# Kernel optimization log

Hardware: AMD Instinct MI355X
Metric: run time of the kernel (lower is better)

## Reference

```python
import jax, jax.numpy as jnp
import numpy as np

DIM = 128
DIM_HEAD = 32
HEADS = 4
EPS = 1e-12  # F.normalize eps


def _l2_normalize(t, axis=-1):
    # matches torch F.normalize(p=2): x / max(||x||, eps)
    n = jnp.sqrt(jnp.sum(t * t, axis=axis, keepdims=True))
    return t / jnp.maximum(n, EPS)


def _dwconv3x3(x_nhwc, k_hwio, c):
    # depthwise 3x3, stride 1, SAME padding, no bias
    return jax.lax.conv_general_dilated(
        x_nhwc, k_hwio, window_strides=(1, 1), padding='SAME',
        dimension_numbers=('NHWC', 'HWIO', 'NHWC'), feature_group_count=c)


def setup_inputs() -> dict:
    key = jax.random.key(0)
    ks = jax.random.split(key, 10)
    b, h, w = 4, 256, 256
    inner = DIM_HEAD * HEADS  # == DIM
    s = 0.02
    return {
        'x': jax.random.normal(ks[0], (b, h, w, DIM), jnp.float32),
        'illumination_feature': jax.random.uniform(ks[1], (b, h, w, inner), jnp.float32),
        'Wq': jax.random.normal(ks[2], (DIM, inner), jnp.float32) * s,  # stored (in,out)
        'Wk': jax.random.normal(ks[3], (DIM, inner), jnp.float32) * s,
        'Wv': jax.random.normal(ks[4], (DIM, inner), jnp.float32) * s,
        'rescale': jnp.ones((HEADS, 1, 1), jnp.float32),
        'Wp': jax.random.normal(ks[5], (inner, DIM), jnp.float32) * s,
        'bp': jnp.zeros((DIM,), jnp.float32),
        'pe_w1': jax.random.normal(ks[6], (3, 3, 1, DIM), jnp.float32) * s,  # HWIO depthwise
        'pe_w2': jax.random.normal(ks[7], (3, 3, 1, DIM), jnp.float32) * s,
    }


def reference(x, illumination_feature, Wq, Wk, Wv, rescale, Wp, bp, pe_w1, pe_w2):
    b, h, w, c = x.shape
    n = h * w
    heads = rescale.shape[0]
    xf = x.reshape(b, n, c)
    ilf = illumination_feature.reshape(b, n, -1)

    q_inp = xf @ Wq  # [b,n,heads*d]
    k_inp = xf @ Wk
    v_inp = xf @ Wv

    def to_heads(t):  # b n (h d) -> b h n d
        return t.reshape(b, n, heads, -1).transpose(0, 2, 1, 3)

    q = to_heads(q_inp)
    k = to_heads(k_inp)
    v = to_heads(v_inp) * to_heads(ilf)  # illumination gating

    # transpose to channel attention layout: b h d n
    q = q.transpose(0, 1, 3, 2)
    k = k.transpose(0, 1, 3, 2)
    v = v.transpose(0, 1, 3, 2)

    q = _l2_normalize(q, axis=-1)
    k = _l2_normalize(k, axis=-1)

    attn = jnp.einsum('bhdn,bhen->bhde', k, q) * rescale  # [b,h,d,d]
    attn = jax.nn.softmax(attn, axis=-1)
    out = jnp.einsum('bhde,bhen->bhdn', attn, v)  # [b,h,d,n]

    # b h d n -> b n (h d)
    out = out.transpose(0, 3, 1, 2).reshape(b, n, -1)
    x1 = (out @ Wp + bp).reshape(b, h, w, c)

    # positional branch: depthwise conv -> GELU -> depthwise conv on v_inp (NHWC)
    v_img = v_inp.reshape(b, h, w, -1)
    x2 = _dwconv3x3(v_img, pe_w1, c)
    x2 = jax.nn.gelu(x2, approximate=False)
    x2 = _dwconv3x3(x2, pe_w2, c)

    return x1 + x2
```

## Files before the change

### kernel.cpp

```cpp
#include <hip/hip_runtime.h>
#include <math.h>

#define B_ 4
#define C_ 128
#define H_ 256
#define W_ 256
#define NPIX (H_*W_)
#define HEADS_ 4

typedef unsigned int uint;
typedef unsigned short ushort;
typedef __attribute__((ext_vector_type(8))) __bf16 bf16x8;
typedef __attribute__((ext_vector_type(4))) float f32x4;

__device__ __forceinline__ ushort f2bf(float f){
    uint u = __builtin_bit_cast(uint, f);
    u += 0x7FFFu + ((u>>16)&1u);
    return (ushort)(u>>16);
}
__device__ __forceinline__ float bf2f(ushort h){
    uint u = ((uint)h)<<16;
    return __builtin_bit_cast(float, u);
}
__device__ __forceinline__ int swz3(int i){ return (i ^ (i>>3)) & 7; }

__global__ __launch_bounds__(256) void k1_syrk(const float* __restrict__ x, float* __restrict__ S){
    __shared__ __align__(16) char sm[128*256];
    int blk = blockIdx.x;
    int b = blk >> 7;
    int chunk = blk & 127;
    long base = ((long)b*NPIX + (long)chunk*512) * C_;
    int t = threadIdx.x;
    int lane = t & 63;
    int w = t >> 6;
    int m0 = (w>>1)*64, n0 = (w&1)*64;

    f32x4 acc[4][4];
    #pragma unroll
    for(int i=0;i<4;i++)
        #pragma unroll
        for(int j=0;j<4;j++) acc[i][j] = {0.f,0.f,0.f,0.f};

    for(int tile=0; tile<4; ++tile){
        {
            int rp = (t>>5)*2;
            int c0 = (t&31)*4;
            const float* xp = x + base + (long)tile*128*C_;
            #pragma unroll
            for(int p=0;p<8;p++){
                int r = p*16 + rp;
                float4 a0 = *(const float4*)(xp + r*C_ + c0);
                float4 a1 = *(const float4*)(xp + (r+1)*C_ + c0);
                float v0[4] = {a0.x,a0.y,a0.z,a0.w};
                float v1[4] = {a1.x,a1.y,a1.z,a1.w};
                #pragma unroll
                for(int i=0;i<4;i++){
                    int cch = c0+i;
                    uint pk = (uint)f2bf(v0[i]) | ((uint)f2bf(v1[i])<<16);
                    *(uint*)(sm + cch*256 + ((2*r) ^ (swz3(cch)<<4))) = pk;
                }
            }
        }
        __syncthreads();
        #pragma unroll
        for(int kk=0;kk<4;kk++){
            int rb = kk*32 + (lane>>4)*8;
            bf16x8 A[4], Bf[4];
            #pragma unroll
            for(int i=0;i<4;i++){
                int cch = m0 + i*16 + (lane&15);
                A[i] = *(const bf16x8*)(sm + cch*256 + ((2*rb) ^ (swz3(cch)<<4)));
            }
            #pragma unroll
            for(int j=0;j<4;j++){
                int cch = n0 + j*16 + (lane&15);
                Bf[j] = *(const bf16x8*)(sm + cch*256 + ((2*rb) ^ (swz3(cch)<<4)));
            }
            #pragma unroll
            for(int i=0;i<4;i++)
                #pragma unroll
                for(int j=0;j<4;j++)
                    acc[i][j] = __builtin_amdgcn_mfma_f32_16x16x32_bf16(A[i], Bf[j], acc[i][j], 0,0,0);
        }
        __syncthreads();
    }
    float* Sb = S + b*C_*C_;
    int rq = (lane>>4)*4;
    int cc = lane&15;
    #pragma unroll
    for(int i=0;i<4;i++)
        #pragma unroll
        for(int j=0;j<4;j++)
            #pragma unroll
            for(int rg=0;rg<4;rg++){
                int row = m0 + i*16 + rq + rg;
                int col = n0 + j*16 + cc;
                atomicAdd(&Sb[row*C_ + col], acc[i][j][rg]);
            }
}

__global__ __launch_bounds__(256) void k2_vinp(const float* __restrict__ x, const float* __restrict__ Wv,
                                               ushort* __restrict__ vout){
    __shared__ __align__(16) char smx[128*256];
    __shared__ __align__(16) char smw[128*256];
    int blk = blockIdx.x;
    int b = blk >> 9; int tileI = blk & 511;
    long rowbase = (long)b*NPIX + (long)tileI*128;
    int t = threadIdx.x, lane = t&63, w = t>>6;
    int m0 = (w>>1)*64, n0 = (w&1)*64;

    {
        #pragma unroll
        for(int p=0;p<16;p++){
            int in = p*8 + (t>>5);
            int o0 = (t&31)*4;
            float4 wv = *(const float4*)(Wv + in*C_ + o0);
            float vv[4]={wv.x,wv.y,wv.z,wv.w};
            #pragma unroll
            for(int i=0;i<4;i++){
                int o = o0+i;
                *(ushort*)(smw + o*256 + ((2*in) ^ (swz3(o)<<4))) = f2bf(vv[i]);
            }
        }
    }
    {
        const float* xp = x + rowbase*C_;
        #pragma unroll
        for(int p=0;p<16;p++){
            int r = p*8 + (t>>5);
            int c0 = (t&31)*4;
            float4 a = *(const float4*)(xp + r*C_ + c0);
            uint2 pk;
            pk.x = (uint)f2bf(a.x) | ((uint)f2bf(a.y)<<16);
            pk.y = (uint)f2bf(a.z) | ((uint)f2bf(a.w)<<16);
            *(uint2*)(smx + r*256 + ((2*c0) ^ (swz3(r)<<4))) = pk;
        }
    }
    __syncthreads();

    f32x4 acc[4][4];
    #pragma unroll
    for(int i=0;i<4;i++)
        #pragma unroll
        for(int j=0;j<4;j++) acc[i][j] = {0.f,0.f,0.f,0.f};

    #pragma unroll
    for(int kk=0;kk<4;kk++){
        int kb = kk*32 + (lane>>4)*8;
        bf16x8 A[4], Bf[4];
        #pragma unroll
        for(int i=0;i<4;i++){
            int r = m0 + i*16 + (lane&15);
            A[i] = *(const bf16x8*)(smx + r*256 + ((2*kb) ^ (swz3(r)<<4)));
        }
        #pragma unroll
        for(int j=0;j<4;j++){
            int o = n0 + j*16 + (lane&15);
            Bf[j] = *(const bf16x8*)(smw + o*256 + ((2*kb) ^ (swz3(o)<<4)));
        }
        #pragma unroll
        for(int i=0;i<4;i++)
            #pragma unroll
            for(int j=0;j<4;j++)
                acc[i][j] = __builtin_amdgcn_mfma_f32_16x16x32_bf16(A[i], Bf[j], acc[i][j], 0,0,0);
    }
    __syncthreads();
    {
        int rq = (lane>>4)*4, cc = lane&15;
        #pragma unroll
        for(int i=0;i<4;i++)
            #pragma unroll
            for(int j=0;j<4;j++)
                #pragma unroll
                for(int rg=0;rg<4;rg++){
                    int row = m0 + i*16 + rq + rg;
                    int col = n0 + j*16 + cc;
                    *(ushort*)(smx + row*256 + ((2*col) ^ (swz3(row)<<4))) = f2bf(acc[i][j][rg]);
                }
    }
    __syncthreads();
    {
        ushort* vp = vout + rowbase*C_;
        #pragma unroll
        for(int p=0;p<8;p++){
            int idx = p*256 + t;
            int row = idx >> 4;
            int ub  = idx & 15;
            uint4 d = *(const uint4*)(smx + row*256 + ((ub*16) ^ (swz3(row)<<4)));
            *(uint4*)(vp + row*C_ + ub*8) = d;
        }
    }
}

__global__ __launch_bounds__(256) void k3a(const float* __restrict__ S, const float* __restrict__ Wq,
                                           const float* __restrict__ Wk, float* __restrict__ TQ,
                                           float* __restrict__ nrm){
    int b = blockIdx.x >> 7, c = blockIdx.x & 127;
    __shared__ float sS[C_];
    int t = threadIdx.x;
    if(t < C_) sS[t] = S[(b*C_+c)*C_ + t];
    __syncthreads();
    const float* Wm = (t < C_) ? Wq : Wk;
    int col = t & (C_-1);
    float acc = 0.f;
    #pragma unroll 4
    for(int c2=0;c2<C_;c2++) acc += sS[c2] * Wm[c2*C_ + col];
    if(t < C_){
        TQ[(b*C_+c)*C_ + col] = acc;
        atomicAdd(&nrm[b*256 + col], Wq[c*C_+col]*acc);
    } else {
        atomicAdd(&nrm[b*256 + C_ + col], Wk[c*C_+col]*acc);
    }
}

__global__ __launch_bounds__(256) void k3b(const float* __restrict__ TQ, const float* __restrict__ Wk,
                                           const float* __restrict__ rescale, const float* __restrict__ Wp,
                                           const float* __restrict__ nrm, ushort* __restrict__ WeffT){
    int b = blockIdx.x >> 2, h = blockIdx.x & 3;
    int t = threadIdx.x;
    __shared__ float sTQ[C_*32];
    __shared__ float sWk[C_*32];
    __shared__ float sG[32*32];
    __shared__ float sinq[32], sink[32];

    #pragma unroll
    for(int p=0;p<16;p++){
        int idx = p*256 + t;
        int c = idx >> 5, e = idx & 31;
        sTQ[idx] = TQ[(b*C_+c)*C_ + h*32 + e];
        sWk[idx] = Wk[c*C_ + h*32 + e];
    }
    if(t < 32) sinq[t] = 1.f/fmaxf(sqrtf(fmaxf(nrm[b*256 + h*32 + t], 0.f)), 1e-12f);
    else if(t < 64) sink[t-32] = 1.f/fmaxf(sqrtf(fmaxf(nrm[b*256 + C_ + h*32 + (t-32)], 0.f)), 1e-12f);
    __syncthreads();

    float g[4];
    #pragma unroll
    for(int p=0;p<4;p++){
        int idx = p*256 + t;
        int d = idx >> 5, e = idx & 31;
        float a = 0.f;
        #pragma unroll 4
        for(int c=0;c<C_;c++) a += sWk[c*32+d]*sTQ[c*32+e];
        g[p] = a;
    }
    #pragma unroll
    for(int p=0;p<4;p++) sG[p*256 + t] = g[p];
    __syncthreads();

    if(t < 32){
        int d = t;
        float rs = rescale[h] * sink[d];
        float l[32]; float mx = -1e30f;
        #pragma unroll
        for(int e=0;e<32;e++){ l[e] = sG[d*32+e]*rs*sinq[e]; mx = fmaxf(mx, l[e]); }
        float sum = 0.f;
        #pragma unroll
        for(int e=0;e<32;e++){ l[e] = expf(l[e]-mx); sum += l[e]; }
        float inv = 1.f/sum;
        #pragma unroll
        for(int e=0;e<32;e++) sG[d*32+e] = l[e]*inv;
    }
    __syncthreads();

    #pragma unroll
    for(int p=0;p<16;p++){
        int idx = p*256 + t;
        int d = idx >> 7, c = idx & 127;
        sTQ[idx] = Wp[(h*32+d)*C_ + c];
    }
    __syncthreads();

    #pragma unroll
    for(int p=0;p<16;p++){
        int idx = p*256 + t;
        int c = idx >> 5, e = idx & 31;
        float a = 0.f;
        #pragma unroll
        for(int d=0;d<32;d++) a += sG[d*32+e]*sTQ[d*128+c];
        WeffT[((long)b*C_+c)*C_ + h*32 + e] = f2bf(a);
    }
}

__global__ __launch_bounds__(256) void k4a_conv1(const ushort* __restrict__ vinp, const float* __restrict__ w1,
                                                 ushort* __restrict__ c1){
    int blk0 = blockIdx.x;
    int blk = (blk0 & 7)*128 + (blk0 >> 3);
    int b = blk >> 8; int y = blk & 255;
    int t = threadIdx.x;
    int c0 = (t & 15)*8;
    int pg = t >> 4;
    float wreg[9][8];
    #pragma unroll
    for(int k=0;k<9;k++){
        float4 a = *(const float4*)(w1 + k*C_ + c0);
        float4 bq = *(const float4*)(w1 + k*C_ + c0 + 4);
        wreg[k][0]=a.x; wreg[k][1]=a.y; wreg[k][2]=a.z; wreg[k][3]=a.w;
        wreg[k][4]=bq.x; wreg[k][5]=bq.y; wreg[k][6]=bq.z; wreg[k][7]=bq.w;
    }
    const ushort* vb = vinp + (long)b*NPIX*C_;
    ushort* cb = c1 + (long)b*NPIX*C_;

    float colA[3][8], colB[3][8], colC[3][8];
    int xbase = pg*16;

    auto loadcol = [&](float (*col)[8], int xcol){
        #pragma unroll
        for(int ky=0;ky<3;ky++){
            int yy = y + ky - 1;
            if(xcol>=0 && xcol<W_ && yy>=0 && yy<H_){
                uint4 vv = *(const uint4*)(vb + ((long)yy*W_ + xcol)*C_ + c0);
                const ushort* pv = (const ushort*)&vv;
                #pragma unroll
                for(int i=0;i<8;i++) col[ky][i] = bf2f(pv[i]);
            } else {
                #pragma unroll
                for(int i=0;i<8;i++) col[ky][i] = 0.f;
            }
        }
    };
    loadcol(colA, xbase-1);
    loadcol(colB, xbase);
    #pragma unroll
    for(int q=0;q<16;q++){
        int xx = xbase + q;
        loadcol(colC, xx+1);
        float s[8];
        #pragma unroll
        for(int i=0;i<8;i++){
            float a = 0.f;
            #pragma unroll
            for(int ky=0;ky<3;ky++){
                a += colA[ky][i]*wreg[ky*3+0][i];
                a += colB[ky][i]*wreg[ky*3+1][i];
                a += colC[ky][i]*wreg[ky*3+2][i];
            }
            s[i] = a;
        }
        uint op[4];
        #pragma unroll
        for(int i2=0;i2<4;i2++){
            float va = s[i2*2],   ga = 0.5f*va*(1.0f+erff(va*0.70710678118654752f));
            float vb2 = s[i2*2+1], gb = 0.5f*vb2*(1.0f+erff(vb2*0.70710678118654752f));
            op[i2] = (uint)f2bf(ga) | ((uint)f2bf(gb)<<16);
        }
        uint4 o; o.x=op[0]; o.y=op[1]; o.z=op[2]; o.w=op[3];
        *(uint4*)(cb + ((long)y*W_ + xx)*C_ + c0) = o;
        #pragma unroll
        for(int ky=0;ky<3;ky++)
            #pragma unroll
            for(int i=0;i<8;i++){ colA[ky][i]=colB[ky][i]; colB[ky][i]=colC[ky][i]; }
    }
}

__global__ __launch_bounds__(256) void k4bc(const ushort* __restrict__ vinp, const float* __restrict__ ilf,
                                            const ushort* __restrict__ WeffT, const float* __restrict__ bp,
                                            const ushort* __restrict__ c1, const float* __restrict__ w2,
                                            float* __restrict__ out){
    __shared__ __align__(16) char smem[65536];
    char* smv = smem;
    char* smw = smem + 32768;
    float* smo = (float*)smem;

    int blk0 = blockIdx.x;
    int blk = (blk0 & 7)*256 + (blk0 >> 3);
    int b = blk >> 9; int tileI = blk & 511;
    long rowbase = (long)b*NPIX + (long)tileI*128;
    int t = threadIdx.x, lane=t&63, w=t>>6;
    int m0=(w>>1)*64, n0=(w&1)*64;
    {
        const ushort* wp = WeffT + b*C_*C_;
        #pragma unroll
        for(int p=0;p<8;p++){
            int idx = p*256 + t;
            int cR = idx >> 4; int ub = idx & 15;
            uint4 d = *(const uint4*)(wp + cR*C_ + ub*8);
            *(uint4*)(smw + cR*256 + ((ub*16) ^ (swz3(cR)<<4))) = d;
        }
    }
    {
        const ushort* vp = vinp + rowbase*C_;
        const float*  ip = ilf + rowbase*C_;
        #pragma unroll
        for(int p=0;p<8;p++){
            int r = p*16 + (t>>4);
            int cl = (t&15)*8;
            uint4 vv = *(const uint4*)(vp + r*C_ + cl);
            const ushort* pv = (const ushort*)&vv;
            float4 i0 = *(const float4*)(ip + r*C_ + cl);
            float4 i1 = *(const float4*)(ip + r*C_ + cl + 4);
            uint4 pk;
            pk.x = (uint)f2bf(bf2f(pv[0])*i0.x) | ((uint)f2bf(bf2f(pv[1])*i0.y)<<16);
            pk.y = (uint)f2bf(bf2f(pv[2])*i0.z) | ((uint)f2bf(bf2f(pv[3])*i0.w)<<16);
            pk.z = (uint)f2bf(bf2f(pv[4])*i1.x) | ((uint)f2bf(bf2f(pv[5])*i1.y)<<16);
            pk.w = (uint)f2bf(bf2f(pv[6])*i1.z) | ((uint)f2bf(bf2f(pv[7])*i1.w)<<16);
            *(uint4*)(smv + r*256 + ((2*cl) ^ (swz3(r)<<4))) = pk;
        }
    }
    __syncthreads();

    f32x4 acc[4][4];
    #pragma unroll
    for(int i=0;i<4;i++)
        #pragma unroll
        for(int j=0;j<4;j++) acc[i][j] = {0.f,0.f,0.f,0.f};

    #pragma unroll
    for(int kk=0;kk<4;kk++){
        int kb = kk*32 + (lane>>4)*8;
        bf16x8 A[4], Bf[4];
        #pragma unroll
        for(int i=0;i<4;i++){
            int r = m0 + i*16 + (lane&15);
            A[i] = *(const bf16x8*)(smv + r*256 + ((2*kb) ^ (swz3(r)<<4)));
        }
        #pragma unroll
        for(int j=0;j<4;j++){
            int o = n0 + j*16 + (lane&15);
            Bf[j] = *(const bf16x8*)(smw + o*256 + ((2*kb) ^ (swz3(o)<<4)));
        }
        #pragma unroll
        for(int i=0;i<4;i++)
            #pragma unroll
            for(int j=0;j<4;j++)
                acc[i][j] = __builtin_amdgcn_mfma_f32_16x16x32_bf16(A[i], Bf[j], acc[i][j], 0,0,0);
    }
    __syncthreads();
    {
        int rq = (lane>>4)*4, cc = lane&15;
        #pragma unroll
        for(int j=0;j<4;j++){
            int col = n0 + j*16 + cc;
            #pragma unroll
            for(int i=0;i<4;i++)
                #pragma unroll
                for(int rg=0;rg<4;rg++){
                    int row = m0 + i*16 + rq + rg;
                    smo[row*C_ + col] = acc[i][j][rg];
                }
        }
    }
    __syncthreads();

    int yt = tileI >> 1;
    int x0 = (tileI & 1) << 7;
    int c0 = (t & 15)*8;
    int pg = t >> 4;
    float wreg[9][8];
    #pragma unroll
    for(int k=0;k<9;k++){
        float4 a = *(const float4*)(w2 + k*C_ + c0);
        float4 bq = *(const float4*)(w2 + k*C_ + c0 + 4);
        wreg[k][0]=a.x; wreg[k][1]=a.y; wreg[k][2]=a.z; wreg[k][3]=a.w;
        wreg[k][4]=bq.x; wreg[k][5]=bq.y; wreg[k][6]=bq.z; wreg[k][7]=bq.w;
    }
    float bias[8];
    {
        float4 b0 = *(const float4*)(bp + c0);
        float4 b1 = *(const float4*)(bp + c0 + 4);
        bias[0]=b0.x; bias[1]=b0.y; bias[2]=b0.z; bias[3]=b0.w;
        bias[4]=b1.x; bias[5]=b1.y; bias[6]=b1.z; bias[7]=b1.w;
    }
    const ushort* cb = c1 + (long)b*NPIX*C_;
    float* ob = out + ((long)b*NPIX + (long)yt*W_)*C_;

    float colA[3][8], colB[3][8], colC[3][8];
    int xbase = x0 + pg*8;

    auto loadcol = [&](float (*col)[8], int xcol){
        #pragma unroll
        for(int ky=0;ky<3;ky++){
            int yy = yt + ky - 1;
            if(xcol>=0 && xcol<W_ && yy>=0 && yy<H_){
                uint4 vv = *(const uint4*)(cb + ((long)yy*W_ + xcol)*C_ + c0);
                const ushort* pv = (const ushort*)&vv;
                #pragma unroll
                for(int i=0;i<8;i++) col[ky][i] = bf2f(pv[i]);
            } else {
                #pragma unroll
                for(int i=0;i<8;i++) col[ky][i] = 0.f;
            }
        }
    };
    loadcol(colA, xbase-1);
    loadcol(colB, xbase);
    #pragma unroll
    for(int q=0;q<8;q++){
        int xx = xbase + q;
        int r  = pg*8 + q;
        loadcol(colC, xx+1);
        float s[8];
        #pragma unroll
        for(int i=0;i<8;i++){
            float a = 0.f;
            #pragma unroll
            for(int ky=0;ky<3;ky++){
                a += colA[ky][i]*wreg[ky*3+0][i];
                a += colB[ky][i]*wreg[ky*3+1][i];
                a += colC[ky][i]*wreg[ky*3+2][i];
            }
            s[i] = a;
        }
        float4 o0, o1;
        o0.x = smo[r*C_ + c0 + 0] + bias[0] + s[0];
        o0.y = smo[r*C_ + c0 + 1] + bias[1] + s[1];
        o0.z = smo[r*C_ + c0 + 2] + bias[2] + s[2];
        o0.w = smo[r*C_ + c0 + 3] + bias[3] + s[3];
        o1.x = smo[r*C_ + c0 + 4] + bias[4] + s[4];
        o1.y = smo[r*C_ + c0 + 5] + bias[5] + s[5];
        o1.z = smo[r*C_ + c0 + 6] + bias[6] + s[6];
        o1.w = smo[r*C_ + c0 + 7] + bias[7] + s[7];
        float* op2 = ob + (long)xx*C_ + c0;
        *(float4*)(op2)     = o0;
        *(float4*)(op2 + 4) = o1;
        #pragma unroll
        for(int ky=0;ky<3;ky++)
            #pragma unroll
            for(int i=0;i<8;i++){ colA[ky][i]=colB[ky][i]; colB[ky][i]=colC[ky][i]; }
    }
}

extern "C" void kernel_launch(void* const* d_in, const int* in_sizes, int n_in,
                              void* d_out, int out_size, void* d_ws, size_t ws_size,
                              hipStream_t stream){
    (void)in_sizes; (void)n_in; (void)out_size; (void)ws_size;
    const float* x    = (const float*)d_in[0];
    const float* ilf  = (const float*)d_in[1];
    const float* Wq   = (const float*)d_in[2];
    const float* Wk   = (const float*)d_in[3];
    const float* Wv   = (const float*)d_in[4];
    const float* rsc  = (const float*)d_in[5];
    const float* Wp   = (const float*)d_in[6];
    const float* bp   = (const float*)d_in[7];
    const float* w1   = (const float*)d_in[8];
    const float* w2   = (const float*)d_in[9];
    float* out = (float*)d_out;
    char* ws = (char*)d_ws;

    ushort* vinp  = (ushort*)ws;
    ushort* c1    = (ushort*)(ws + 67108864);
    float*  TQ    = (float*)(ws + 67108864);
    float*  S     = (float*)(ws + 134217728);
    float*  nrm   = (float*)(ws + 134479872);
    ushort* WeffT = (ushort*)(ws + 134483968);

    hipMemsetAsync(S, 0, 262144 + 4096, stream);
    hipLaunchKernelGGL(k1_syrk,  dim3(512),  dim3(256), 0, stream, x, S);
    hipLaunchKernelGGL(k2_vinp,  dim3(2048), dim3(256), 0, stream, x, Wv, vinp);
    hipLaunchKernelGGL(k3a,      dim3(512),  dim3(256), 0, stream, S, Wq, Wk, TQ, nrm);
    hipLaunchKernelGGL(k3b,      dim3(16),   dim3(256), 0, stream, TQ, Wk, rsc, Wp, nrm, WeffT);
    hipLaunchKernelGGL(k4a_conv1,dim3(1024), dim3(256), 0, stream, vinp, w1, c1);
    hipLaunchKernelGGL(k4bc,     dim3(2048), dim3(256), 0, stream, vinp, ilf, WeffT, bp, c1, w2, out);
}
```

Measured before the change: 344.2 us.

## Fuse Gram and v_inp projection kernels; hold weights in registers; 512-thread blocks

Merges the x^T x Gram accumulation and the x@Wv projection into one kernel so x is read from HBM once instead of twice. Each tile is staged in LDS in both row-major and transposed bf16 layouts. Wv fragments, and WeffT fragments in k4bc, now live in registers instead of LDS. Both kernels move to 512-thread blocks with 8 waves, and the k4bc output staging gets a swizzled fp32 LDS layout read as float4. The cost is more registers and extra LDS writes and barriers per tile, which may lower occupancy.

```diff
diff --git a/kernel.cpp b/kernel.cpp
--- a/kernel.cpp
+++ b/kernel.cpp
@@ -22,24 +22,41 @@
     uint u = ((uint)h)<<16;
     return __builtin_bit_cast(float, u);
 }
+__device__ __forceinline__ __bf16 f2bfv(float f){
+    return __builtin_bit_cast(__bf16, f2bf(f));
+}
 __device__ __forceinline__ int swz3(int i){ return (i ^ (i>>3)) & 7; }
 
-__global__ __launch_bounds__(256) void k1_syrk(const float* __restrict__ x, float* __restrict__ S){
-    __shared__ __align__(16) char sm[128*256];
+__global__ __launch_bounds__(512) void k12(const float* __restrict__ x, const float* __restrict__ Wv,
+                                           float* __restrict__ S, ushort* __restrict__ vinp){
+    __shared__ __align__(16) char smX[32768];
+    __shared__ __align__(16) char smT[32768];
     int blk = blockIdx.x;
-    int b = blk >> 7;
-    int chunk = blk & 127;
+    int b = blk >> 7, chunk = blk & 127;
     long base = ((long)b*NPIX + (long)chunk*512) * C_;
-    int t = threadIdx.x;
-    int lane = t & 63;
-    int w = t >> 6;
-    int m0 = (w>>1)*64, n0 = (w&1)*64;
-
-    f32x4 acc[4][4];
+    int t = threadIdx.x, lane = t & 63, w = t >> 6;
+    int wm = w >> 2, wn = w & 3;
+    int m0 = wm*64, n0 = wn*32;
+
+    bf16x8 Bv[4][2];
+    #pragma unroll
+    for(int kk=0;kk<4;kk++){
+        int kb = kk*32 + (lane>>4)*8;
+        #pragma unroll
+        for(int j=0;j<2;j++){
+            int col = n0 + j*16 + (lane&15);
+            bf16x8 v;
+            #pragma unroll
+            for(int jj=0;jj<8;jj++) v[jj] = f2bfv(Wv[(kb+jj)*C_ + col]);
+            Bv[kk][j] = v;
+        }
+    }
+
+    f32x4 acc_s[4][2];
     #pragma unroll
     for(int i=0;i<4;i++)
         #pragma unroll
-        for(int j=0;j<4;j++) acc[i][j] = {0.f,0.f,0.f,0.f};
+        for(int j=0;j<2;j++) acc_s[i][j] = {0.f,0.f,0.f,0.f};
 
     for(int tile=0; tile<4; ++tile){
         {
@@ -47,149 +64,105 @@
             int c0 = (t&31)*4;
             const float* xp = x + base + (long)tile*128*C_;
             #pragma unroll
-            for(int p=0;p<8;p++){
-                int r = p*16 + rp;
+            for(int p=0;p<4;p++){
+                int r = p*32 + rp;
                 float4 a0 = *(const float4*)(xp + r*C_ + c0);
                 float4 a1 = *(const float4*)(xp + (r+1)*C_ + c0);
-                float v0[4] = {a0.x,a0.y,a0.z,a0.w};
-                float v1[4] = {a1.x,a1.y,a1.z,a1.w};
+                ushort h0[4] = {f2bf(a0.x), f2bf(a0.y), f2bf(a0.z), f2bf(a0.w)};
+                ushort h1[4] = {f2bf(a1.x), f2bf(a1.y), f2bf(a1.z), f2bf(a1.w)};
+                uint2 pk0, pk1;
+                pk0.x = (uint)h0[0] | ((uint)h0[1]<<16);
+                pk0.y = (uint)h0[2] | ((uint)h0[3]<<16);
+                pk1.x = (uint)h1[0] | ((uint)h1[1]<<16);
+                pk1.y = (uint)h1[2] | ((uint)h1[3]<<16);
+                *(uint2*)(smX + r*256     + ((2*c0) ^ (swz3(r)<<4)))   = pk0;
+                *(uint2*)(smX + (r+1)*256 + ((2*c0) ^ (swz3(r+1)<<4))) = pk1;
                 #pragma unroll
                 for(int i=0;i<4;i++){
-                    int cch = c0+i;
-                    uint pk = (uint)f2bf(v0[i]) | ((uint)f2bf(v1[i])<<16);
-                    *(uint*)(sm + cch*256 + ((2*r) ^ (swz3(cch)<<4))) = pk;
+                    int ch = c0+i;
+                    uint pk = (uint)h0[i] | ((uint)h1[i]<<16);
+                    *(uint*)(smT + ch*256 + ((2*r) ^ (swz3(ch)<<4))) = pk;
                 }
             }
         }
         __syncthreads();
+
+        f32x4 acc_v[4][2];
+        #pragma unroll
+        for(int i=0;i<4;i++)
+            #pragma unroll
+            for(int j=0;j<2;j++) acc_v[i][j] = {0.f,0.f,0.f,0.f};
+
         #pragma unroll
         for(int kk=0;kk<4;kk++){
-            int rb = kk*32 + (lane>>4)*8;
-            bf16x8 A[4], Bf[4];
+            int kb = kk*32 + (lane>>4)*8;
+            bf16x8 A[4];
             #pragma unroll
             for(int i=0;i<4;i++){
-                int cch = m0 + i*16 + (lane&15);
-                A[i] = *(const bf16x8*)(sm + cch*256 + ((2*rb) ^ (swz3(cch)<<4)));
-            }
-            #pragma unroll
-            for(int j=0;j<4;j++){
-                int cch = n0 + j*16 + (lane&15);
-                Bf[j] = *(const bf16x8*)(sm + cch*256 + ((2*rb) ^ (swz3(cch)<<4)));
+                int r = m0 + i*16 + (lane&15);
+                A[i] = *(const bf16x8*)(smX + r*256 + ((2*kb) ^ (swz3(r)<<4)));
             }
             #pragma unroll
             for(int i=0;i<4;i++)
                 #pragma unroll
-                for(int j=0;j<4;j++)
-                    acc[i][j] = __builtin_amdgcn_mfma_f32_16x16x32_bf16(A[i], Bf[j], acc[i][j], 0,0,0);
+                for(int j=0;j<2;j++)
+                    acc_v[i][j] = __builtin_amdgcn_mfma_f32_16x16x32_bf16(A[i], Bv[kk][j], acc_v[i][j], 0,0,0);
+            bf16x8 As[4], Bs[2];
+            #pragma unroll
+            for(int i=0;i<4;i++){
+                int ch = m0 + i*16 + (lane&15);
+                As[i] = *(const bf16x8*)(smT + ch*256 + ((2*kb) ^ (swz3(ch)<<4)));
+            }
+            #pragma unroll
+            for(int j=0;j<2;j++){
+                int ch = n0 + j*16 + (lane&15);
+                Bs[j] = *(const bf16x8*)(smT + ch*256 + ((2*kb) ^ (swz3(ch)<<4)));
+            }
+            #pragma unroll
+            for(int i=0;i<4;i++)
+                #pragma unroll
+                for(int j=0;j<2;j++)
+                    acc_s[i][j] = __builtin_amdgcn_mfma_f32_16x16x32_bf16(As[i], Bs[j], acc_s[i][j], 0,0,0);
         }
         __syncthreads();
+        {
+            int rq = (lane>>4)*4, cc = lane&15;
+            #pragma unroll
+            for(int i=0;i<4;i++)
+                #pragma unroll
+                for(int j=0;j<2;j++)
+                    #pragma unroll
+                    for(int rg=0;rg<4;rg++){
+                        int row = m0 + i*16 + rq + rg;
+                        int col = n0 + j*16 + cc;
+                        *(ushort*)(smX + row*256 + ((2*col) ^ (swz3(row)<<4))) = f2bf(acc_v[i][j][rg]);
+                    }
+        }
+        __syncthreads();
+        {
+            long off = base + (long)tile*128*C_;
+            #pragma unroll
+            for(int p=0;p<4;p++){
+                int idx = p*512 + t;
+                int row = idx >> 4, ub = idx & 15;
+                uint4 d = *(const uint4*)(smX + row*256 + ((ub*16) ^ (swz3(row)<<4)));
+                *(uint4*)(vinp + off + row*C_ + ub*8) = d;
+            }
+        }
+        __syncthreads();
     }
     float* Sb = S + b*C_*C_;
-    int rq = (lane>>4)*4;
-    int cc = lane&15;
+    int rq = (lane>>4)*4, cc = lane&15;
     #pragma unroll
     for(int i=0;i<4;i++)
         #pragma unroll
-        for(int j=0;j<4;j++)
+        for(int j=0;j<2;j++)
             #pragma unroll
             for(int rg=0;rg<4;rg++){
                 int row = m0 + i*16 + rq + rg;
                 int col = n0 + j*16 + cc;
-                atomicAdd(&Sb[row*C_ + col], acc[i][j][rg]);
-            }
-}
-
-__global__ __launch_bounds__(256) void k2_vinp(const float* __restrict__ x, const float* __restrict__ Wv,
-                                               ushort* __restrict__ vout){
-    __shared__ __align__(16) char smx[128*256];
-    __shared__ __align__(16) char smw[128*256];
-    int blk = blockIdx.x;
-    int b = blk >> 9; int tileI = blk & 511;
-    long rowbase = (long)b*NPIX + (long)tileI*128;
-    int t = threadIdx.x, lane = t&63, w = t>>6;
-    int m0 = (w>>1)*64, n0 = (w&1)*64;
-
-    {
-        #pragma unroll
-        for(int p=0;p<16;p++){
-            int in = p*8 + (t>>5);
-            int o0 = (t&31)*4;
-            float4 wv = *(const float4*)(Wv + in*C_ + o0);
-            float vv[4]={wv.x,wv.y,wv.z,wv.w};
-            #pragma unroll
-            for(int i=0;i<4;i++){
-                int o = o0+i;
-                *(ushort*)(smw + o*256 + ((2*in) ^ (swz3(o)<<4))) = f2bf(vv[i]);
-            }
-        }
-    }
-    {
-        const float* xp = x + rowbase*C_;
-        #pragma unroll
-        for(int p=0;p<16;p++){
-            int r = p*8 + (t>>5);
-            int c0 = (t&31)*4;
-            float4 a = *(const float4*)(xp + r*C_ + c0);
-            uint2 pk;
-            pk.x = (uint)f2bf(a.x) | ((uint)f2bf(a.y)<<16);
-            pk.y = (uint)f2bf(a.z) | ((uint)f2bf(a.w)<<16);
-            *(uint2*)(smx + r*256 + ((2*c0) ^ (swz3(r)<<4))) = pk;
-        }
-    }
-    __syncthreads();
-
-    f32x4 acc[4][4];
-    #pragma unroll
-    for(int i=0;i<4;i++)
-        #pragma unroll
-        for(int j=0;j<4;j++) acc[i][j] = {0.f,0.f,0.f,0.f};
-
-    #pragma unroll
-    for(int kk=0;kk<4;kk++){
-        int kb = kk*32 + (lane>>4)*8;
-        bf16x8 A[4], Bf[4];
-        #pragma unroll
-        for(int i=0;i<4;i++){
-            int r = m0 + i*16 + (lane&15);
-            A[i] = *(const bf16x8*)(smx + r*256 + ((2*kb) ^ (swz3(r)<<4)));
-        }
-        #pragma unroll
-        for(int j=0;j<4;j++){
-            int o = n0 + j*16 + (lane&15);
-            Bf[j] = *(const bf16x8*)(smw + o*256 + ((2*kb) ^ (swz3(o)<<4)));
-        }
-        #pragma unroll
-        for(int i=0;i<4;i++)
-            #pragma unroll
-            for(int j=0;j<4;j++)
-                acc[i][j] = __builtin_amdgcn_mfma_f32_16x16x32_bf16(A[i], Bf[j], acc[i][j], 0,0,0);
-    }
-    __syncthreads();
-    {
-        int rq = (lane>>4)*4, cc = lane&15;
-        #pragma unroll
-        for(int i=0;i<4;i++)
-            #pragma unroll
-            for(int j=0;j<4;j++)
-                #pragma unroll
-                for(int rg=0;rg<4;rg++){
-                    int row = m0 + i*16 + rq + rg;
-                    int col = n0 + j*16 + cc;
-                    *(ushort*)(smx + row*256 + ((2*col) ^ (swz3(row)<<4))) = f2bf(acc[i][j][rg]);
-                }
-    }
-    __syncthreads();
-    {
-        ushort* vp = vout + rowbase*C_;
-        #pragma unroll
-        for(int p=0;p<8;p++){
-            int idx = p*256 + t;
-            int row = idx >> 4;
-            int ub  = idx & 15;
-            uint4 d = *(const uint4*)(smx + row*256 + ((ub*16) ^ (swz3(row)<<4)));
-            *(uint4*)(vp + row*C_ + ub*8) = d;
-        }
-    }
+                atomicAdd(&Sb[row*C_ + col], acc_s[i][j][rg]);
+            }
 }
 
 __global__ __launch_bounds__(256) void k3a(const float* __restrict__ S, const float* __restrict__ Wq,
@@ -353,38 +326,43 @@
     }
 }
 
-__global__ __launch_bounds__(256) void k4bc(const ushort* __restrict__ vinp, const float* __restrict__ ilf,
+__global__ __launch_bounds__(512) void k4bc(const ushort* __restrict__ vinp, const float* __restrict__ ilf,
                                             const ushort* __restrict__ WeffT, const float* __restrict__ bp,
                                             const ushort* __restrict__ c1, const float* __restrict__ w2,
                                             float* __restrict__ out){
     __shared__ __align__(16) char smem[65536];
     char* smv = smem;
-    char* smw = smem + 32768;
-    float* smo = (float*)smem;
+    char* smo = smem;
 
     int blk0 = blockIdx.x;
     int blk = (blk0 & 7)*256 + (blk0 >> 3);
     int b = blk >> 9; int tileI = blk & 511;
     long rowbase = (long)b*NPIX + (long)tileI*128;
-    int t = threadIdx.x, lane=t&63, w=t>>6;
-    int m0=(w>>1)*64, n0=(w&1)*64;
+    int t = threadIdx.x, lane = t&63, w = t>>6;
+    int wm = w>>2, wn = w&3;
+    int m0 = wm*64, n0 = wn*32;
+
+    bf16x8 Bw[4][2];
     {
         const ushort* wp = WeffT + b*C_*C_;
         #pragma unroll
-        for(int p=0;p<8;p++){
-            int idx = p*256 + t;
-            int cR = idx >> 4; int ub = idx & 15;
-            uint4 d = *(const uint4*)(wp + cR*C_ + ub*8);
-            *(uint4*)(smw + cR*256 + ((ub*16) ^ (swz3(cR)<<4))) = d;
+        for(int kk=0;kk<4;kk++){
+            int kb = kk*32 + (lane>>4)*8;
+            #pragma unroll
+            for(int j=0;j<2;j++){
+                int col = n0 + j*16 + (lane&15);
+                Bw[kk][j] = *(const bf16x8*)(wp + col*C_ + kb);
+            }
         }
     }
     {
         const ushort* vp = vinp + rowbase*C_;
         const float*  ip = ilf + rowbase*C_;
         #pragma unroll
-        for(int p=0;p<8;p++){
-            int r = p*16 + (t>>4);
-            int cl = (t&15)*8;
+        for(int p=0;p<4;p++){
+            int idx = p*512 + t;
+            int r = idx >> 4;
+            int cl = (idx & 15)*8;
             uint4 vv = *(const uint4*)(vp + r*C_ + cl);
             const ushort* pv = (const ushort*)&vv;
             float4 i0 = *(const float4*)(ip + r*C_ + cl);
@@ -399,46 +377,40 @@
     }
     __syncthreads();
 
-    f32x4 acc[4][4];
+    f32x4 acc[4][2];
     #pragma unroll
     for(int i=0;i<4;i++)
         #pragma unroll
-        for(int j=0;j<4;j++) acc[i][j] = {0.f,0.f,0.f,0.f};
+        for(int j=0;j<2;j++) acc[i][j] = {0.f,0.f,0.f,0.f};
 
     #pragma unroll
     for(int kk=0;kk<4;kk++){
         int kb = kk*32 + (lane>>4)*8;
-        bf16x8 A[4], Bf[4];
+        bf16x8 A[4];
         #pragma unroll
         for(int i=0;i<4;i++){
             int r = m0 + i*16 + (lane&15);
             A[i] = *(const bf16x8*)(smv + r*256 + ((2*kb) ^ (swz3(r)<<4)));
         }
         #pragma unroll
-        for(int j=0;j<4;j++){
-            int o = n0 + j*16 + (lane&15);
-            Bf[j] = *(const bf16x8*)(smw + o*256 + ((2*kb) ^ (swz3(o)<<4)));
-        }
-        #pragma unroll
         for(int i=0;i<4;i++)
             #pragma unroll
-            for(int j=0;j<4;j++)
-                acc[i][j] = __builtin_amdgcn_mfma_f32_16x16x32_bf16(A[i], Bf[j], acc[i][j], 0,0,0);
+            for(int j=0;j<2;j++)
+                acc[i][j] = __builtin_amdgcn_mfma_f32_16x16x32_bf16(A[i], Bw[kk][j], acc[i][j], 0,0,0);
     }
     __syncthreads();
     {
         int rq = (lane>>4)*4, cc = lane&15;
         #pragma unroll
-        for(int j=0;j<4;j++){
-            int col = n0 + j*16 + cc;
-            #pragma unroll
-            for(int i=0;i<4;i++)
+        for(int i=0;i<4;i++)
+            #pragma unroll
+            for(int j=0;j<2;j++)
                 #pragma unroll
                 for(int rg=0;rg<4;rg++){
                     int row = m0 + i*16 + rq + rg;
-                    smo[row*C_ + col] = acc[i][j][rg];
+                    int col = n0 + j*16 + cc;
+                    *(float*)(smo + row*512 + ((col*4) ^ (swz3(row)<<4))) = acc[i][j][rg];
                 }
-        }
     }
     __syncthreads();
 
@@ -465,7 +437,7 @@
     float* ob = out + ((long)b*NPIX + (long)yt*W_)*C_;
 
     float colA[3][8], colB[3][8], colC[3][8];
-    int xbase = x0 + pg*8;
+    int xbase = x0 + pg*4;
 
     auto loadcol = [&](float (*col)[8], int xcol){
         #pragma unroll
@@ -485,9 +457,9 @@
     loadcol(colA, xbase-1);
     loadcol(colB, xbase);
     #pragma unroll
-    for(int q=0;q<8;q++){
+    for(int q=0;q<4;q++){
         int xx = xbase + q;
-        int r  = pg*8 + q;
+        int r  = pg*4 + q;
         loadcol(colC, xx+1);
         float s[8];
         #pragma unroll
@@ -501,15 +473,17 @@
             }
             s[i] = a;
         }
+        float4 m0v = *(const float4*)(smo + r*512 + (((c0  )*4) ^ (swz3(r)<<4)));
+        float4 m1v = *(const float4*)(smo + r*512 + (((c0+4)*4) ^ (swz3(r)<<4)));
         float4 o0, o1;
-        o0.x = smo[r*C_ + c0 + 0] + bias[0] + s[0];
-        o0.y = smo[r*C_ + c0 + 1] + bias[1] + s[1];
-        o0.z = smo[r*C_ + c0 + 2] + bias[2] + s[2];
-        o0.w = smo[r*C_ + c0 + 3] + bias[3] + s[3];
-        o1.x = smo[r*C_ + c0 + 4] + bias[4] + s[4];
-        o1.y = smo[r*C_ + c0 + 5] + bias[5] + s[5];
-        o1.z = smo[r*C_ + c0 + 6] + bias[6] + s[6];
-        o1.w = smo[r*C_ + c0 + 7] + bias[7] + s[7];
+        o0.x = m0v.x + bias[0] + s[0];
+        o0.y = m0v.y + bias[1] + s[1];
+        o0.z = m0v.z + bias[2] + s[2];
+        o0.w = m0v.w + bias[3] + s[3];
+        o1.x = m1v.x + bias[4] + s[4];
+        o1.y = m1v.y + bias[5] + s[5];
+        o1.z = m1v.z + bias[6] + s[6];
+        o1.w = m1v.w + bias[7] + s[7];
         float* op2 = ob + (long)xx*C_ + c0;
         *(float4*)(op2)     = o0;
         *(float4*)(op2 + 4) = o1;
@@ -545,10 +519,9 @@
     ushort* WeffT = (ushort*)(ws + 134483968);
 
     hipMemsetAsync(S, 0, 262144 + 4096, stream);
-    hipLaunchKernelGGL(k1_syrk,  dim3(512),  dim3(256), 0, stream, x, S);
-    hipLaunchKernelGGL(k2_vinp,  dim3(2048), dim3(256), 0, stream, x, Wv, vinp);
+    hipLaunchKernelGGL(k12,      dim3(512),  dim3(512), 0, stream, x, Wv, S, vinp);
     hipLaunchKernelGGL(k3a,      dim3(512),  dim3(256), 0, stream, S, Wq, Wk, TQ, nrm);
     hipLaunchKernelGGL(k3b,      dim3(16),   dim3(256), 0, stream, TQ, Wk, rsc, Wp, nrm, WeffT);
     hipLaunchKernelGGL(k4a_conv1,dim3(1024), dim3(256), 0, stream, vinp, w1, c1);
-    hipLaunchKernelGGL(k4bc,     dim3(2048), dim3(256), 0, stream, vinp, ilf, WeffT, bp, c1, w2, out);
-}
+    hipLaunchKernelGGL(k4bc,     dim3(2048), dim3(512), 0, stream, vinp, ilf, WeffT, bp, c1, w2, out);
+}
```

Measured after the change: 309.8 us. 1.11x faster.
